# Optimization experiments

Measured on AMD Instinct MI355X. Metric: run time of the kernel, lower is better.

## Reference

```python
import jax, jax.numpy as jnp
import numpy as np

B, T, F_DIM, HID, CH = 16, 4096, 47, 64, 256  # batch, frames, feature_dim, hidden_feature_dim, num_channels


def setup_inputs() -> dict:
    key = jax.random.key(0)
    ks = jax.random.split(key, 8)
    s = 0.08  # weight scale
    return {
        "features": jax.random.normal(ks[0], (B, T, F_DIM), jnp.float32),
        # conv1: Conv1d(47, 64, k=1) -> pointwise linear, torch weight (out,in,1) squeezed
        "W1": jax.random.normal(ks[1], (HID, F_DIM), jnp.float32) * s,
        "b1": jnp.zeros((HID,), jnp.float32),
        # conv2: Conv1d(256, 256, k=2), torch weight (out, in, k)
        "W2": jax.random.normal(ks[2], (CH, 4 * HID, 2), jnp.float32) * s,
        "b2": jnp.zeros((CH,), jnp.float32),
        # tconv: ConvTranspose1d(256, 256, k=4, stride=4), torch weight (in, out, k)
        "Wt": jax.random.normal(ks[3], (CH, CH, 4), jnp.float32) * s,
        "bt": jnp.zeros((CH,), jnp.float32),
        # GRU(256, 256), torch layout: (3*H, in) with gate order [r, z, n]
        "W_ih": jax.random.normal(ks[4], (3 * CH, CH), jnp.float32) * s,
        "W_hh": jax.random.normal(ks[5], (3 * CH, CH), jnp.float32) * s,
        "b_ih": jnp.zeros((3 * CH,), jnp.float32),
        "b_hh": jnp.zeros((3 * CH,), jnp.float32),
    }


def reference(features, W1, b1, W2, b2, Wt, bt, W_ih, W_hh, b_ih, b_hh):
    b, t = features.shape[0], features.shape[1]
    ch = Wt.shape[1]
    # conv1 (k=1) == pointwise linear + tanh: (B,T,47) -> (B,T,64)
    c = jnp.tanh(jnp.einsum('btf,hf->bth', features, W1) + b1)
    # group 4 frames: (B, T/4, 256)
    c = c.reshape(b, t // 4, -1)
    # conv2 k=2 with left pad 1 (causal): y[t] = W2[..0] x[t-1] + W2[..1] x[t]
    cp = jnp.pad(c, ((0, 0), (1, 0), (0, 0)))
    c = jnp.tanh(jnp.einsum('bti,oi->bto', cp[:, :-1], W2[:, :, 0])
                 + jnp.einsum('bti,oi->bto', cp[:, 1:], W2[:, :, 1]) + b2)
    # tconv: stride-4 transpose conv, k=4 -> each frame emits 4 steps
    c = jnp.tanh(jnp.einsum('bti,iok->btko', c, Wt) + bt)  # (B, T/4, 4, CH)
    c = c.reshape(b, t, ch)
    # GRU (torch semantics, gate order r,z,n); precompute input projections
    gates_x = jnp.einsum('btc,gc->btg', c, W_ih) + b_ih  # (B,T,3CH)

    def step(h, gx):
        gh = h @ W_hh.T + b_hh
        xr, xz, xn = jnp.split(gx, 3, axis=-1)
        hr, hz, hn = jnp.split(gh, 3, axis=-1)
        r = jax.nn.sigmoid(xr + hr)
        z = jax.nn.sigmoid(xz + hz)
        n = jnp.tanh(xn + r * hn)
        h = (1 - z) * n + z * h
        return h, h

    h0 = jnp.zeros((b, ch), features.dtype)
    _, hs = jax.lax.scan(step, h0, jnp.swapaxes(gates_x, 0, 1))  # (T,B,CH)
    return jnp.swapaxes(hs, 0, 1)  # (B,T,CH)
```

## Files before the change

### kernel.cpp

```cpp
#include <hip/hip_runtime.h>
#include <hip/hip_bf16.h>
#include <stdint.h>

#define B_   16
#define T_   4096
#define F_   47
#define HID_ 64
#define CH_  256
#define TG_  1024
#define G3_  768

using bf16x8 = __attribute__((ext_vector_type(8))) short;
using f32x4  = __attribute__((ext_vector_type(4))) float;
using f16x8  = __attribute__((ext_vector_type(8))) _Float16;
using h2     = __attribute__((ext_vector_type(2))) _Float16;

__device__ __forceinline__ short f2bf(float f) {
    union { float f; uint32_t u; } v; v.f = f;
    uint32_t u = v.u;
    uint32_t r = (u + 0x7fffu + ((u >> 16) & 1u)) >> 16;
    return (short)r;
}
__device__ __forceinline__ float bf2f(short s) {
    union { uint32_t u; float f; } v; v.u = ((uint32_t)(uint16_t)s) << 16;
    return v.f;
}
__device__ __forceinline__ float fast_tanh(float x) {
    float e = __expf(2.f * x);
    return 1.f - 2.f / (e + 1.f);
}
__device__ __forceinline__ float fast_sigmoid(float x) {
    return 1.f / (1.f + __expf(-x));
}

#if __has_builtin(__builtin_amdgcn_fdot2)
#define FDOT2(a, b, c) __builtin_amdgcn_fdot2((a), (b), (c), false)
#else
__device__ __forceinline__ float fdot2_emul(h2 a, h2 b, float c) {
    return c + (float)a[0] * (float)b[0] + (float)a[1] * (float)b[1];
}
#define FDOT2(a, b, c) fdot2_emul((a), (b), (c))
#endif

#if __has_builtin(__builtin_amdgcn_global_load_lds)
#define HAS_GLL 1
__device__ __forceinline__ void gl_lds16(const void* g, void* l) {
    __builtin_amdgcn_global_load_lds(
        (const __attribute__((address_space(1))) uint32_t*)g,
        (__attribute__((address_space(3))) uint32_t*)l, 16, 0, 0);
}
#else
#define HAS_GLL 0
#endif

__global__ __launch_bounds__(256) void k1_conv1(const float* __restrict__ feat,
        const float* __restrict__ W1, const float* __restrict__ b1,
        short* __restrict__ c1) {
    __shared__ float sW[47 * 64];
    __shared__ float sF[4 * 47];
    int tid = threadIdx.x;
    int b = blockIdx.x >> 10, t0 = (blockIdx.x & 1023) * 4;
    if (tid < 188) sF[tid] = feat[((size_t)b * T_ + t0) * 47 + tid];
    for (int i = tid; i < 47 * 64; i += 256) {
        int f = i >> 6, h = i & 63;
        sW[i] = W1[h * 47 + f];
    }
    __syncthreads();
    int fr = tid >> 6, h = tid & 63;
    float acc = b1[h];
    #pragma unroll
    for (int f = 0; f < 47; ++f)
        acc += sF[fr * 47 + f] * sW[f * 64 + h];
    c1[((size_t)b * T_ + t0 + fr) * 64 + h] = f2bf(fast_tanh(acc));
}

__global__ __launch_bounds__(256) void k_prep(const float* __restrict__ W2,
        const float* __restrict__ Wt, const float* __restrict__ Wih_f,
        short* __restrict__ W2t, short* __restrict__ Wtt, short* __restrict__ Wih) {
    int idx = blockIdx.x * 256 + threadIdx.x;
    if (idx < 256 * 512) {
        int o = idx >> 9, i = idx & 511, d = i >> 8, jj = i & 255;
        W2t[idx] = f2bf(W2[(size_t)o * 512 + jj * 2 + d]);
    }
    {
        int n = idx >> 8, ic = idx & 255, o = n & 255, kp = n >> 8;
        Wtt[idx] = f2bf(Wt[(size_t)ic * 1024 + o * 4 + kp]);
    }
    if (idx < G3_ * CH_)
        Wih[idx] = f2bf(Wih_f[idx]);
}

__global__ __launch_bounds__(256) void k2_conv2(const short* __restrict__ c1,
        const short* __restrict__ W2t, const float* __restrict__ b2,
        short* __restrict__ y2) {
    int tid = threadIdx.x, w = tid >> 6, l = tid & 63;
    int lane16 = l & 15, quad = l >> 4;
    int mt = blockIdx.x * 4 + w;
    int row = mt * 16 + lane16;
    int tg = row & 1023;
    const short* Arow = c1 + (size_t)row * 256 - 256;
    bf16x8 zero8 = {0,0,0,0,0,0,0,0};
    bf16x8 af[16];
    #pragma unroll
    for (int kt = 0; kt < 16; ++kt) {
        int i0 = kt * 32 + quad * 8;
        bool masked = (tg == 0) && (kt < 8);
        const short* p = masked ? c1 : (Arow + i0);
        bf16x8 v = *(const bf16x8*)p;
        af[kt] = masked ? zero8 : v;
    }
    #pragma unroll
    for (int nt = 0; nt < 16; ++nt) {
        int n = nt * 16 + lane16;
        f32x4 acc = {0.f, 0.f, 0.f, 0.f};
        const short* Brow = W2t + (size_t)n * 512 + quad * 8;
        #pragma unroll
        for (int kt = 0; kt < 16; ++kt) {
            bf16x8 bf = *(const bf16x8*)(Brow + kt * 32);
            acc = __builtin_amdgcn_mfma_f32_16x16x32_bf16(af[kt], bf, acc, 0, 0, 0);
        }
        float bias = b2[n];
        #pragma unroll
        for (int r = 0; r < 4; ++r) {
            int mrow = mt * 16 + quad * 4 + r;
            y2[(size_t)mrow * 256 + n] = f2bf(fast_tanh(acc[r] + bias));
        }
    }
}

__global__ __launch_bounds__(256) void k3a_tconv(const short* __restrict__ y2,
        const short* __restrict__ Wtt, const float* __restrict__ bt,
        short* __restrict__ c3) {
    int tid = threadIdx.x, w = tid >> 6, l = tid & 63;
    int lane16 = l & 15, quad = l >> 4;
    int mt = blockIdx.x;
    int row = mt * 16 + lane16;
    const short* Arow = y2 + (size_t)row * 256 + quad * 8;
    bf16x8 af[8];
    #pragma unroll
    for (int kt = 0; kt < 8; ++kt) af[kt] = *(const bf16x8*)(Arow + kt * 32);
    #pragma unroll
    for (int nt2 = 0; nt2 < 16; ++nt2) {
        int n = (w * 16 + nt2) * 16 + lane16;
        f32x4 acc = {0.f, 0.f, 0.f, 0.f};
        const short* Brow = Wtt + (size_t)n * 256 + quad * 8;
        #pragma unroll
        for (int kt = 0; kt < 8; ++kt) {
            bf16x8 bf = *(const bf16x8*)(Brow + kt * 32);
            acc = __builtin_amdgcn_mfma_f32_16x16x32_bf16(af[kt], bf, acc, 0, 0, 0);
        }
        int kp = n >> 8, o = n & 255;
        float bias = bt[o];
        #pragma unroll
        for (int r = 0; r < 4; ++r) {
            int mrow = mt * 16 + quad * 4 + r;
            int bb = mrow >> 10, tgg = mrow & 1023;
            c3[(((size_t)bb * TG_ + tgg) * 4 + kp) * 256 + o] =
                f2bf(fast_tanh(acc[r] + bias));
        }
    }
}

__global__ __launch_bounds__(256) void k3b_xproj(const short* __restrict__ c3,
        const short* __restrict__ Wih, const float* __restrict__ b_ih,
        short* __restrict__ gates) {
    int tid = threadIdx.x, w = tid >> 6, l = tid & 63;
    int lane16 = l & 15, quad = l >> 4;
    int mt = blockIdx.x;
    int row = mt * 16 + lane16;
    const short* Arow = c3 + (size_t)row * 256 + quad * 8;
    bf16x8 af[8];
    #pragma unroll
    for (int kt = 0; kt < 8; ++kt) af[kt] = *(const bf16x8*)(Arow + kt * 32);
    #pragma unroll
    for (int nt2 = 0; nt2 < 12; ++nt2) {
        int n = (w * 12 + nt2) * 16 + lane16;
        f32x4 acc = {0.f, 0.f, 0.f, 0.f};
        const short* Brow = Wih + (size_t)n * 256 + quad * 8;
        #pragma unroll
        for (int kt = 0; kt < 8; ++kt) {
            bf16x8 bf = *(const bf16x8*)(Brow + kt * 32);
            acc = __builtin_amdgcn_mfma_f32_16x16x32_bf16(af[kt], bf, acc, 0, 0, 0);
        }
        float bias = b_ih[n];
        #pragma unroll
        for (int r = 0; r < 4; ++r) {
            int mrow = mt * 16 + quad * 4 + r;
            gates[(size_t)mrow * G3_ + n] = f2bf(acc[r] + bias);
        }
    }
}

__global__ __launch_bounds__(512) void k4_gru_dot2(const float* __restrict__ W_hh,
        const float* __restrict__ b_hh, const short* __restrict__ gates,
        float* __restrict__ out) {
    __shared__ __align__(16) short gxb[2][8][G3_];
    __shared__ __align__(16) float part[G3_ * 4];
    __shared__ __align__(16) float ob[8 * 256];
    __shared__ __align__(16) short hq_s[4 * 72];

    int tid = threadIdx.x, l = tid & 63, w = tid >> 6;
    int q = tid & 3, n0 = tid >> 2;
    int b = blockIdx.x;

    h2 wreg[6][32];
    #pragma unroll
    for (int k = 0; k < 6; ++k) {
        const float2* row = (const float2*)(W_hh + ((size_t)(n0 + k * 128)) * 256 + q * 64);
        #pragma unroll
        for (int j = 0; j < 32; ++j) {
            float2 v = row[j];
            h2 p; p[0] = (_Float16)v.x; p[1] = (_Float16)v.y;
            wreg[k][j] = p;
        }
    }

    float h_reg = 0.f, bhr = 0.f, bhz = 0.f, bhn = 0.f;
    if (tid < 256) {
        bhr = b_hh[tid]; bhz = b_hh[256 + tid]; bhn = b_hh[512 + tid];
    }
    if (tid < 288) hq_s[tid] = 0;

    const short* gbase = gates + (size_t)b * T_ * G3_;
    const char* gbytes = (const char*)gbase;

#if HAS_GLL
    {
        char* dst = (char*)&gxb[0][0][0];
        gl_lds16(gbytes + w * 1024 + l * 16, dst + w * 1024);
        if (w < 4) gl_lds16(gbytes + (8 + w) * 1024 + l * 16, dst + (8 + w) * 1024);
    }
#else
    {
        const uint32_t* g32 = (const uint32_t*)gbytes;
        uint32_t* d = (uint32_t*)&gxb[0][0][0];
        #pragma unroll
        for (int i = 0; i < 6; ++i) d[tid + i * 512] = g32[tid + i * 512];
    }
#endif
    __syncthreads();

    float* outb = out + (size_t)b * T_ * CH_;
    for (int s = 0; s < T_; ++s) {
        bool grp0 = ((s & 7) == 0) && (s + 8 < T_);
#if HAS_GLL
        if (grp0) {
            const char* src = gbytes + (size_t)(s + 8) * 1536;
            char* dst = (char*)&gxb[((s >> 3) + 1) & 1][0][0];
            gl_lds16(src + w * 1024 + l * 16, dst + w * 1024);
            if (w < 4) gl_lds16(src + (8 + w) * 1024 + l * 16, dst + (8 + w) * 1024);
        }
#else
        uint32_t pf[6];
        if (grp0) {
            const uint32_t* src = (const uint32_t*)(gbytes + (size_t)(s + 8) * 1536);
            #pragma unroll
            for (int i = 0; i < 6; ++i) pf[i] = src[tid + i * 512];
        }
#endif

        h2 hq[32];
        #pragma unroll
        for (int g2 = 0; g2 < 8; ++g2) {
            f16x8 v = *(const f16x8*)&hq_s[q * 72 + g2 * 8];
            #pragma unroll
            for (int p2 = 0; p2 < 4; ++p2) {
                h2 p; p[0] = v[p2 * 2]; p[1] = v[p2 * 2 + 1];
                hq[g2 * 4 + p2] = p;
            }
        }
        float acc[6] = {0.f, 0.f, 0.f, 0.f, 0.f, 0.f};
        #pragma unroll
        for (int j = 0; j < 32; ++j) {
            #pragma unroll
            for (int k = 0; k < 6; ++k)
                acc[k] = FDOT2(wreg[k][j], hq[j], acc[k]);
        }
        #pragma unroll
        for (int k = 0; k < 6; ++k)
            part[(n0 + k * 128) * 4 + q] = acc[k];
        __syncthreads();

#if !HAS_GLL
        if (grp0) {
            uint32_t* d = (uint32_t*)&gxb[((s >> 3) + 1) & 1][0][0];
            #pragma unroll
            for (int i = 0; i < 6; ++i) d[tid + i * 512] = pf[i];
        }
#endif
        if (tid < 256) {
            const short* gx = &gxb[(s >> 3) & 1][s & 7][0];
            f32x4 pr = *(const f32x4*)&part[tid * 4];
            f32x4 pz = *(const f32x4*)&part[(256 + tid) * 4];
            f32x4 pn = *(const f32x4*)&part[(512 + tid) * 4];
            float gr = (pr[0] + pr[1]) + (pr[2] + pr[3]);
            float gz = (pz[0] + pz[1]) + (pz[2] + pz[3]);
            float gn = (pn[0] + pn[1]) + (pn[2] + pn[3]);
            float xr = bf2f(gx[tid]), xz = bf2f(gx[256 + tid]), xn = bf2f(gx[512 + tid]);
            float r = fast_sigmoid(xr + gr + bhr);
            float z = fast_sigmoid(xz + gz + bhz);
            float nn = fast_tanh(xn + r * (gn + bhn));
            h_reg = (1.f - z) * nn + z * h_reg;
            union { _Float16 f; short u; } cv; cv.f = (_Float16)h_reg;
            hq_s[(tid >> 6) * 72 + (tid & 63)] = cv.u;
            ob[(s & 7) * 256 + tid] = h_reg;
        }
        __syncthreads();

        if ((s & 7) == 7) {
            f32x4 v = *(const f32x4*)&ob[tid * 4];
            *(f32x4*)&outb[(size_t)(s - 7 + (tid >> 6)) * 256 + (tid & 63) * 4] = v;
        }
    }
}

extern "C" void kernel_launch(void* const* d_in, const int* in_sizes, int n_in,
                              void* d_out, int out_size, void* d_ws, size_t ws_size,
                              hipStream_t stream) {
    const float* feat  = (const float*)d_in[0];
    const float* W1    = (const float*)d_in[1];
    const float* b1    = (const float*)d_in[2];
    const float* W2    = (const float*)d_in[3];
    const float* b2    = (const float*)d_in[4];
    const float* Wt    = (const float*)d_in[5];
    const float* bt    = (const float*)d_in[6];
    const float* Wih_f = (const float*)d_in[7];
    const float* Whh   = (const float*)d_in[8];
    const float* bih   = (const float*)d_in[9];
    const float* bhh   = (const float*)d_in[10];
    float* out = (float*)d_out;

    char* ws = (char*)d_ws;
    short* c3    = (short*)(ws);
    short* c1    = (short*)(ws);
    short* gates = (short*)(ws + 33554432);
    short* y2    = (short*)(ws + 33554432);
    short* W2t   = (short*)(ws + 134217728);
    short* Wtt   = (short*)(ws + 134217728 + 262144);
    short* Wih   = (short*)(ws + 134217728 + 262144 + 524288);

    k1_conv1   <<<16384, 256, 0, stream>>>(feat, W1, b1, c1);
    k_prep     <<<1024, 256, 0, stream>>>(W2, Wt, Wih_f, W2t, Wtt, Wih);
    k2_conv2   <<<256,  256, 0, stream>>>(c1, W2t, b2, y2);
    k3a_tconv  <<<1024, 256, 0, stream>>>(y2, Wtt, bt, c3);
    k3b_xproj  <<<4096, 256, 0, stream>>>(c3, Wih, bih, gates);
    k4_gru_dot2<<<16,   512, 0, stream>>>(Whh, bhh, gates, out);
}
```

Measured before the change: 5.216 ms.

## Replace GRU recurrent fdot2 matvec with MFMA f16 using broadcast hidden state

The per-step recurrent matvec W_hh·h in the GRU kernel now uses 16x16x32 f16 MFMA instructions instead of per-thread fdot2 partial sums. The weight fragments stay in registers and the hidden vector is broadcast as the B operand, so only one column of each result tile is used. This removes the 4-way partial-sum reduction through shared memory and lowers instruction count on the serial critical path. In exchange, 15/16 of the MFMA output is wasted and MFMA latency is added on every step, and launch_bounds(512,2) caps registers per thread.

Measured after the change: 5.763 ms. 1.1x slower.

```diff
diff --git a/kernel.cpp b/kernel.cpp
--- a/kernel.cpp
+++ b/kernel.cpp
@@ -13,7 +13,6 @@
 using bf16x8 = __attribute__((ext_vector_type(8))) short;
 using f32x4  = __attribute__((ext_vector_type(4))) float;
 using f16x8  = __attribute__((ext_vector_type(8))) _Float16;
-using h2     = __attribute__((ext_vector_type(2))) _Float16;
 
 __device__ __forceinline__ short f2bf(float f) {
     union { float f; uint32_t u; } v; v.f = f;
@@ -32,15 +31,6 @@
 __device__ __forceinline__ float fast_sigmoid(float x) {
     return 1.f / (1.f + __expf(-x));
 }
-
-#if __has_builtin(__builtin_amdgcn_fdot2)
-#define FDOT2(a, b, c) __builtin_amdgcn_fdot2((a), (b), (c), false)
-#else
-__device__ __forceinline__ float fdot2_emul(h2 a, h2 b, float c) {
-    return c + (float)a[0] * (float)b[0] + (float)a[1] * (float)b[1];
-}
-#define FDOT2(a, b, c) fdot2_emul((a), (b), (c))
-#endif
 
 #if __has_builtin(__builtin_amdgcn_global_load_lds)
 #define HAS_GLL 1
@@ -191,35 +181,40 @@
     }
 }
 
-__global__ __launch_bounds__(512) void k4_gru_dot2(const float* __restrict__ W_hh,
+__global__ __launch_bounds__(512, 2) void k4_gru_mfma(const float* __restrict__ W_hh,
         const float* __restrict__ b_hh, const short* __restrict__ gates,
         float* __restrict__ out) {
     __shared__ __align__(16) short gxb[2][8][G3_];
-    __shared__ __align__(16) float part[G3_ * 4];
+    __shared__ __align__(16) float part[G3_];
     __shared__ __align__(16) float ob[8 * 256];
-    __shared__ __align__(16) short hq_s[4 * 72];
+    __shared__ __align__(16) _Float16 h_s[256];
 
     int tid = threadIdx.x, l = tid & 63, w = tid >> 6;
-    int q = tid & 3, n0 = tid >> 2;
+    int lane16 = l & 15, quad = l >> 4;
     int b = blockIdx.x;
 
-    h2 wreg[6][32];
-    #pragma unroll
-    for (int k = 0; k < 6; ++k) {
-        const float2* row = (const float2*)(W_hh + ((size_t)(n0 + k * 128)) * 256 + q * 64);
-        #pragma unroll
-        for (int j = 0; j < 32; ++j) {
-            float2 v = row[j];
-            h2 p; p[0] = (_Float16)v.x; p[1] = (_Float16)v.y;
-            wreg[k][j] = p;
+    f16x8 frag[6][8];
+    #pragma unroll
+    for (int mt = 0; mt < 6; ++mt) {
+        const float* wrow = W_hh + (size_t)((w * 6 + mt) * 16 + lane16) * 256 + quad * 8;
+        #pragma unroll
+        for (int kt = 0; kt < 8; ++kt) {
+            const float4* p = (const float4*)(wrow + kt * 32);
+            float4 x = p[0], y = p[1];
+            f16x8 f;
+            f[0] = (_Float16)x.x; f[1] = (_Float16)x.y;
+            f[2] = (_Float16)x.z; f[3] = (_Float16)x.w;
+            f[4] = (_Float16)y.x; f[5] = (_Float16)y.y;
+            f[6] = (_Float16)y.z; f[7] = (_Float16)y.w;
+            frag[mt][kt] = f;
         }
     }
 
     float h_reg = 0.f, bhr = 0.f, bhz = 0.f, bhn = 0.f;
     if (tid < 256) {
         bhr = b_hh[tid]; bhz = b_hh[256 + tid]; bhn = b_hh[512 + tid];
-    }
-    if (tid < 288) hq_s[tid] = 0;
+        h_s[tid] = (_Float16)0.f;
+    }
 
     const short* gbase = gates + (size_t)b * T_ * G3_;
     const char* gbytes = (const char*)gbase;
@@ -259,26 +254,21 @@
         }
 #endif
 
-        h2 hq[32];
-        #pragma unroll
-        for (int g2 = 0; g2 < 8; ++g2) {
-            f16x8 v = *(const f16x8*)&hq_s[q * 72 + g2 * 8];
+        f32x4 acc[6];
+        #pragma unroll
+        for (int mt = 0; mt < 6; ++mt) acc[mt] = (f32x4){0.f, 0.f, 0.f, 0.f};
+        #pragma unroll
+        for (int kt = 0; kt < 8; ++kt) {
+            f16x8 hb = *(const f16x8*)&h_s[kt * 32 + quad * 8];
             #pragma unroll
-            for (int p2 = 0; p2 < 4; ++p2) {
-                h2 p; p[0] = v[p2 * 2]; p[1] = v[p2 * 2 + 1];
-                hq[g2 * 4 + p2] = p;
-            }
-        }
-        float acc[6] = {0.f, 0.f, 0.f, 0.f, 0.f, 0.f};
-        #pragma unroll
-        for (int j = 0; j < 32; ++j) {
+            for (int mt = 0; mt < 6; ++mt)
+                acc[mt] = __builtin_amdgcn_mfma_f32_16x16x32_f16(frag[mt][kt], hb, acc[mt], 0, 0, 0);
+        }
+        if (lane16 == 0) {
             #pragma unroll
-            for (int k = 0; k < 6; ++k)
-                acc[k] = FDOT2(wreg[k][j], hq[j], acc[k]);
-        }
-        #pragma unroll
-        for (int k = 0; k < 6; ++k)
-            part[(n0 + k * 128) * 4 + q] = acc[k];
+            for (int mt = 0; mt < 6; ++mt)
+                *(f32x4*)&part[(w * 6 + mt) * 16 + quad * 4] = acc[mt];
+        }
         __syncthreads();
 
 #if !HAS_GLL
@@ -290,19 +280,15 @@
 #endif
         if (tid < 256) {
             const short* gx = &gxb[(s >> 3) & 1][s & 7][0];
-            f32x4 pr = *(const f32x4*)&part[tid * 4];
-            f32x4 pz = *(const f32x4*)&part[(256 + tid) * 4];
-            f32x4 pn = *(const f32x4*)&part[(512 + tid) * 4];
-            float gr = (pr[0] + pr[1]) + (pr[2] + pr[3]);
-            float gz = (pz[0] + pz[1]) + (pz[2] + pz[3]);
-            float gn = (pn[0] + pn[1]) + (pn[2] + pn[3]);
+            float gr = part[tid];
+            float gz = part[256 + tid];
+            float gn = part[512 + tid];
             float xr = bf2f(gx[tid]), xz = bf2f(gx[256 + tid]), xn = bf2f(gx[512 + tid]);
             float r = fast_sigmoid(xr + gr + bhr);
             float z = fast_sigmoid(xz + gz + bhz);
             float nn = fast_tanh(xn + r * (gn + bhn));
             h_reg = (1.f - z) * nn + z * h_reg;
-            union { _Float16 f; short u; } cv; cv.f = (_Float16)h_reg;
-            hq_s[(tid >> 6) * 72 + (tid & 63)] = cv.u;
+            h_s[tid] = (_Float16)h_reg;
             ob[(s & 7) * 256 + tid] = h_reg;
         }
         __syncthreads();
@@ -344,5 +330,5 @@
     k2_conv2   <<<256,  256, 0, stream>>>(c1, W2t, b2, y2);
     k3a_tconv  <<<1024, 256, 0, stream>>>(y2, Wtt, bt, c3);
     k3b_xproj  <<<4096, 256, 0, stream>>>(c3, Wih, bih, gates);
-    k4_gru_dot2<<<16,   512, 0, stream>>>(Whh, bhh, gates, out);
-}
+    k4_gru_mfma<<<16,   512, 0, stream>>>(Whh, bhh, gates, out);
+}
```

## Reduce GRU partial sums with DPP and drop one barrier per step

Applied to the files above, without the earlier changes.

The GRU recurrence kernel used to write per-quad partial dot products to shared memory, synchronise, and then have 256 threads sum them. Now the four partials are combined with DPP cross-lane adds inside each quad, and each gate lane pair directly computes the hidden update for its own channel. The hidden-state and output staging buffers are double-buffered so only one __syncthreads per timestep remains. The recurrent bias is folded into the accumulator init, and launch bounds ask for two blocks per CU, which may limit the registers available for the weight arrays held in registers.

After: 5.393 ms. 1.03x slower.

```diff
diff --git a/kernel.cpp b/kernel.cpp
--- a/kernel.cpp
+++ b/kernel.cpp
@@ -41,6 +41,14 @@
 }
 #define FDOT2(a, b, c) fdot2_emul((a), (b), (c))
 #endif
+
+template <int CTRL>
+__device__ __forceinline__ float dpp_add(float x) {
+    union { float f; int i; } a, b;
+    a.f = x;
+    b.i = __builtin_amdgcn_update_dpp(0, a.i, CTRL, 0xf, 0xf, true);
+    return x + b.f;
+}
 
 #if __has_builtin(__builtin_amdgcn_global_load_lds)
 #define HAS_GLL 1
@@ -191,13 +199,12 @@
     }
 }
 
-__global__ __launch_bounds__(512) void k4_gru_dot2(const float* __restrict__ W_hh,
+__global__ __launch_bounds__(512, 2) void k4_gru_dot2(const float* __restrict__ W_hh,
         const float* __restrict__ b_hh, const short* __restrict__ gates,
         float* __restrict__ out) {
     __shared__ __align__(16) short gxb[2][8][G3_];
-    __shared__ __align__(16) float part[G3_ * 4];
-    __shared__ __align__(16) float ob[8 * 256];
-    __shared__ __align__(16) short hq_s[4 * 72];
+    __shared__ __align__(16) float ob[2][8 * 256];
+    __shared__ __align__(16) short hq_s[2][4 * 72];
 
     int tid = threadIdx.x, l = tid & 63, w = tid >> 6;
     int q = tid & 3, n0 = tid >> 2;
@@ -215,11 +222,15 @@
         }
     }
 
-    float h_reg = 0.f, bhr = 0.f, bhz = 0.f, bhn = 0.f;
-    if (tid < 256) {
-        bhr = b_hh[tid]; bhz = b_hh[256 + tid]; bhn = b_hh[512 + tid];
-    }
-    if (tid < 288) hq_s[tid] = 0;
+    float bh[6];
+    #pragma unroll
+    for (int k = 0; k < 6; ++k)
+        bh[k] = (q == 0) ? b_hh[n0 + k * 128] : 0.f;
+
+    float h_reg = 0.f;
+    int c = n0 + (q & 1) * 128;
+
+    if (tid < 288) hq_s[0][tid] = 0;
 
     const short* gbase = gates + (size_t)b * T_ * G3_;
     const char* gbytes = (const char*)gbase;
@@ -259,27 +270,27 @@
         }
 #endif
 
-        h2 hq[32];
+        float acc[6];
+        #pragma unroll
+        for (int k = 0; k < 6; ++k) acc[k] = bh[k];
+        const short* hb = &hq_s[s & 1][q * 72];
         #pragma unroll
         for (int g2 = 0; g2 < 8; ++g2) {
-            f16x8 v = *(const f16x8*)&hq_s[q * 72 + g2 * 8];
+            f16x8 v = *(const f16x8*)(hb + g2 * 8);
             #pragma unroll
             for (int p2 = 0; p2 < 4; ++p2) {
-                h2 p; p[0] = v[p2 * 2]; p[1] = v[p2 * 2 + 1];
-                hq[g2 * 4 + p2] = p;
+                h2 hv; hv[0] = v[p2 * 2]; hv[1] = v[p2 * 2 + 1];
+                #pragma unroll
+                for (int k = 0; k < 6; ++k)
+                    acc[k] = FDOT2(wreg[k][g2 * 4 + p2], hv, acc[k]);
             }
         }
-        float acc[6] = {0.f, 0.f, 0.f, 0.f, 0.f, 0.f};
-        #pragma unroll
-        for (int j = 0; j < 32; ++j) {
-            #pragma unroll
-            for (int k = 0; k < 6; ++k)
-                acc[k] = FDOT2(wreg[k][j], hq[j], acc[k]);
-        }
-        #pragma unroll
-        for (int k = 0; k < 6; ++k)
-            part[(n0 + k * 128) * 4 + q] = acc[k];
-        __syncthreads();
+
+        #pragma unroll
+        for (int k = 0; k < 6; ++k) {
+            acc[k] = dpp_add<0xB1>(acc[k]);
+            acc[k] = dpp_add<0x4E>(acc[k]);
+        }
 
 #if !HAS_GLL
         if (grp0) {
@@ -288,27 +299,24 @@
             for (int i = 0; i < 6; ++i) d[tid + i * 512] = pf[i];
         }
 #endif
-        if (tid < 256) {
+        if (q < 2) {
             const short* gx = &gxb[(s >> 3) & 1][s & 7][0];
-            f32x4 pr = *(const f32x4*)&part[tid * 4];
-            f32x4 pz = *(const f32x4*)&part[(256 + tid) * 4];
-            f32x4 pn = *(const f32x4*)&part[(512 + tid) * 4];
-            float gr = (pr[0] + pr[1]) + (pr[2] + pr[3]);
-            float gz = (pz[0] + pz[1]) + (pz[2] + pz[3]);
-            float gn = (pn[0] + pn[1]) + (pn[2] + pn[3]);
-            float xr = bf2f(gx[tid]), xz = bf2f(gx[256 + tid]), xn = bf2f(gx[512 + tid]);
-            float r = fast_sigmoid(xr + gr + bhr);
-            float z = fast_sigmoid(xz + gz + bhz);
-            float nn = fast_tanh(xn + r * (gn + bhn));
+            float gr = (q & 1) ? acc[1] : acc[0];
+            float gz = (q & 1) ? acc[3] : acc[2];
+            float gn = (q & 1) ? acc[5] : acc[4];
+            float xr = bf2f(gx[c]), xz = bf2f(gx[256 + c]), xn = bf2f(gx[512 + c]);
+            float r = fast_sigmoid(xr + gr);
+            float z = fast_sigmoid(xz + gz);
+            float nn = fast_tanh(xn + r * gn);
             h_reg = (1.f - z) * nn + z * h_reg;
             union { _Float16 f; short u; } cv; cv.f = (_Float16)h_reg;
-            hq_s[(tid >> 6) * 72 + (tid & 63)] = cv.u;
-            ob[(s & 7) * 256 + tid] = h_reg;
+            hq_s[(s + 1) & 1][(c >> 6) * 72 + (c & 63)] = cv.u;
+            ob[(s >> 3) & 1][(s & 7) * 256 + c] = h_reg;
         }
         __syncthreads();
 
         if ((s & 7) == 7) {
-            f32x4 v = *(const f32x4*)&ob[tid * 4];
+            f32x4 v = *(const f32x4*)&ob[(s >> 3) & 1][tid * 4];
             *(f32x4*)&outb[(size_t)(s - 7 + (tid >> 6)) * 256 + (tid & 63) * 4] = v;
         }
     }
```

## Double GRU block to 1024 threads, reduce dot partials via DPP, double-buffer h

Applied to the files above, without the earlier changes.

The recurrent GRU kernel now runs 1024 threads per batch element, so each thread holds 3 weight rows' quarter-slices instead of 6, which halves per-thread dot work and register pressure. The four partial sums per output are combined with DPP cross-lane adds rather than written to LDS and summed by the gate threads. The half-precision hidden state is double-buffered so the next step's writes do not race with this step's reads. The cost is more waves per block and wider barriers on every one of the 4096 serial steps.

Measured after the change: 5.822 ms. +11.6%, slower.

```diff
diff --git a/kernel.cpp b/kernel.cpp
--- a/kernel.cpp
+++ b/kernel.cpp
@@ -41,6 +41,14 @@
 }
 #define FDOT2(a, b, c) fdot2_emul((a), (b), (c))
 #endif
+
+template <int CTRL>
+__device__ __forceinline__ float dpp_add(float x) {
+    union { float f; int i; } a, b;
+    a.f = x;
+    b.i = __builtin_amdgcn_update_dpp(0, a.i, CTRL, 0xf, 0xf, true);
+    return x + b.f;
+}
 
 #if __has_builtin(__builtin_amdgcn_global_load_lds)
 #define HAS_GLL 1
@@ -191,22 +199,22 @@
     }
 }
 
-__global__ __launch_bounds__(512) void k4_gru_dot2(const float* __restrict__ W_hh,
+__global__ __launch_bounds__(1024) void k4_gru_dot2(const float* __restrict__ W_hh,
         const float* __restrict__ b_hh, const short* __restrict__ gates,
         float* __restrict__ out) {
     __shared__ __align__(16) short gxb[2][8][G3_];
-    __shared__ __align__(16) float part[G3_ * 4];
+    __shared__ __align__(16) float part[G3_];
     __shared__ __align__(16) float ob[8 * 256];
-    __shared__ __align__(16) short hq_s[4 * 72];
+    __shared__ __align__(16) short hq_s[2][4 * 72];
 
     int tid = threadIdx.x, l = tid & 63, w = tid >> 6;
     int q = tid & 3, n0 = tid >> 2;
     int b = blockIdx.x;
 
-    h2 wreg[6][32];
-    #pragma unroll
-    for (int k = 0; k < 6; ++k) {
-        const float2* row = (const float2*)(W_hh + ((size_t)(n0 + k * 128)) * 256 + q * 64);
+    h2 wreg[3][32];
+    #pragma unroll
+    for (int k = 0; k < 3; ++k) {
+        const float2* row = (const float2*)(W_hh + ((size_t)(n0 + k * 256)) * 256 + q * 64);
         #pragma unroll
         for (int j = 0; j < 32; ++j) {
             float2 v = row[j];
@@ -219,23 +227,22 @@
     if (tid < 256) {
         bhr = b_hh[tid]; bhz = b_hh[256 + tid]; bhn = b_hh[512 + tid];
     }
-    if (tid < 288) hq_s[tid] = 0;
+    if (tid < 288) hq_s[0][tid] = 0;
 
     const short* gbase = gates + (size_t)b * T_ * G3_;
     const char* gbytes = (const char*)gbase;
 
 #if HAS_GLL
-    {
+    if (w < 12) {
         char* dst = (char*)&gxb[0][0][0];
         gl_lds16(gbytes + w * 1024 + l * 16, dst + w * 1024);
-        if (w < 4) gl_lds16(gbytes + (8 + w) * 1024 + l * 16, dst + (8 + w) * 1024);
     }
 #else
     {
         const uint32_t* g32 = (const uint32_t*)gbytes;
         uint32_t* d = (uint32_t*)&gxb[0][0][0];
         #pragma unroll
-        for (int i = 0; i < 6; ++i) d[tid + i * 512] = g32[tid + i * 512];
+        for (int i = 0; i < 3; ++i) d[tid + i * 1024] = g32[tid + i * 1024];
     }
 #endif
     __syncthreads();
@@ -244,70 +251,68 @@
     for (int s = 0; s < T_; ++s) {
         bool grp0 = ((s & 7) == 0) && (s + 8 < T_);
 #if HAS_GLL
-        if (grp0) {
+        if (grp0 && w < 12) {
             const char* src = gbytes + (size_t)(s + 8) * 1536;
             char* dst = (char*)&gxb[((s >> 3) + 1) & 1][0][0];
             gl_lds16(src + w * 1024 + l * 16, dst + w * 1024);
-            if (w < 4) gl_lds16(src + (8 + w) * 1024 + l * 16, dst + (8 + w) * 1024);
         }
 #else
-        uint32_t pf[6];
+        uint32_t pf[3];
         if (grp0) {
             const uint32_t* src = (const uint32_t*)(gbytes + (size_t)(s + 8) * 1536);
             #pragma unroll
-            for (int i = 0; i < 6; ++i) pf[i] = src[tid + i * 512];
-        }
-#endif
-
-        h2 hq[32];
+            for (int i = 0; i < 3; ++i) pf[i] = src[tid + i * 1024];
+        }
+#endif
+
+        float acc0 = 0.f, acc1 = 0.f, acc2 = 0.f;
+        const short* hb = &hq_s[s & 1][q * 72];
         #pragma unroll
         for (int g2 = 0; g2 < 8; ++g2) {
-            f16x8 v = *(const f16x8*)&hq_s[q * 72 + g2 * 8];
+            f16x8 v = *(const f16x8*)(hb + g2 * 8);
             #pragma unroll
             for (int p2 = 0; p2 < 4; ++p2) {
-                h2 p; p[0] = v[p2 * 2]; p[1] = v[p2 * 2 + 1];
-                hq[g2 * 4 + p2] = p;
+                h2 hv; hv[0] = v[p2 * 2]; hv[1] = v[p2 * 2 + 1];
+                acc0 = FDOT2(wreg[0][g2 * 4 + p2], hv, acc0);
+                acc1 = FDOT2(wreg[1][g2 * 4 + p2], hv, acc1);
+                acc2 = FDOT2(wreg[2][g2 * 4 + p2], hv, acc2);
             }
         }
-        float acc[6] = {0.f, 0.f, 0.f, 0.f, 0.f, 0.f};
-        #pragma unroll
-        for (int j = 0; j < 32; ++j) {
-            #pragma unroll
-            for (int k = 0; k < 6; ++k)
-                acc[k] = FDOT2(wreg[k][j], hq[j], acc[k]);
-        }
-        #pragma unroll
-        for (int k = 0; k < 6; ++k)
-            part[(n0 + k * 128) * 4 + q] = acc[k];
+
+        acc0 = dpp_add<0xB1>(acc0); acc0 = dpp_add<0x4E>(acc0);
+        acc1 = dpp_add<0xB1>(acc1); acc1 = dpp_add<0x4E>(acc1);
+        acc2 = dpp_add<0xB1>(acc2); acc2 = dpp_add<0x4E>(acc2);
+        if (q == 0) {
+            part[n0]       = acc0;
+            part[256 + n0] = acc1;
+            part[512 + n0] = acc2;
+        }
         __syncthreads();
 
 #if !HAS_GLL
         if (grp0) {
             uint32_t* d = (uint32_t*)&gxb[((s >> 3) + 1) & 1][0][0];
             #pragma unroll
-            for (int i = 0; i < 6; ++i) d[tid + i * 512] = pf[i];
+            for (int i = 0; i < 3; ++i) d[tid + i * 1024] = pf[i];
         }
 #endif
         if (tid < 256) {
             const short* gx = &gxb[(s >> 3) & 1][s & 7][0];
-            f32x4 pr = *(const f32x4*)&part[tid * 4];
-            f32x4 pz = *(const f32x4*)&part[(256 + tid) * 4];
-            f32x4 pn = *(const f32x4*)&part[(512 + tid) * 4];
-            float gr = (pr[0] + pr[1]) + (pr[2] + pr[3]);
-            float gz = (pz[0] + pz[1]) + (pz[2] + pz[3]);
-            float gn = (pn[0] + pn[1]) + (pn[2] + pn[3]);
+            float gr = part[tid];
+            float gz = part[256 + tid];
+            float gn = part[512 + tid];
             float xr = bf2f(gx[tid]), xz = bf2f(gx[256 + tid]), xn = bf2f(gx[512 + tid]);
             float r = fast_sigmoid(xr + gr + bhr);
             float z = fast_sigmoid(xz + gz + bhz);
             float nn = fast_tanh(xn + r * (gn + bhn));
             h_reg = (1.f - z) * nn + z * h_reg;
             union { _Float16 f; short u; } cv; cv.f = (_Float16)h_reg;
-            hq_s[(tid >> 6) * 72 + (tid & 63)] = cv.u;
+            hq_s[(s + 1) & 1][(tid >> 6) * 72 + (tid & 63)] = cv.u;
             ob[(s & 7) * 256 + tid] = h_reg;
         }
         __syncthreads();
 
-        if ((s & 7) == 7) {
+        if ((s & 7) == 7 && tid < 512) {
             f32x4 v = *(const f32x4*)&ob[tid * 4];
             *(f32x4*)&outb[(size_t)(s - 7 + (tid >> 6)) * 256 + (tid & 63) * 4] = v;
         }
@@ -344,5 +349,5 @@
     k2_conv2   <<<256,  256, 0, stream>>>(c1, W2t, b2, y2);
     k3a_tconv  <<<1024, 256, 0, stream>>>(y2, Wtt, bt, c3);
     k3b_xproj  <<<4096, 256, 0, stream>>>(c3, Wih, bih, gates);
-    k4_gru_dot2<<<16,   512, 0, stream>>>(Whh, bhh, gates, out);
-}
+    k4_gru_dot2<<<16,   1024, 0, stream>>>(Whh, bhh, gates, out);
+}
```
